# Optimization experiments

Measured on AMD Instinct MI355X. Metric: run time of the kernel, lower is better.

The kernel has to match this reference:

```python
import jax, jax.numpy as jnp
import numpy as np

H = 12        # num_heads
BLOCK = 128   # sliding-window block_size (include_adjacent=True)
EPS = 1e-5


def layer_norm(x, s, b):
    m = x.mean(-1, keepdims=True)
    v = ((x - m) ** 2).mean(-1, keepdims=True)
    return (x - m) * jax.lax.rsqrt(v + EPS) * s + b


def setup_inputs() -> dict:
    key = jax.random.key(0)
    V, D, F, L, B, S, C = 32000, 768, 3072, 4, 8, 1024, 2
    ks = jax.random.split(key, 10)
    r = lambda k, shp: jax.random.normal(k, shp, dtype=jnp.float32) * 0.02
    return {
        "tokens": jax.random.randint(ks[0], (B, S), 0, V),
        "mask": jnp.ones((B, S), dtype=jnp.int32),
        "emb": r(ks[1], (V, D)),
        "in_w": r(ks[2], (L, 3 * D, D)),
        "in_b": jnp.zeros((L, 3 * D), jnp.float32),
        "out_w": r(ks[3], (L, D, D)),
        "out_b": jnp.zeros((L, D), jnp.float32),
        "ln1_s": jnp.ones((L, D), jnp.float32),
        "ln1_b": jnp.zeros((L, D), jnp.float32),
        "ln2_s": jnp.ones((L, D), jnp.float32),
        "ln2_b": jnp.zeros((L, D), jnp.float32),
        "ff_w1": r(ks[4], (L, F, D)),
        "ff_b1": jnp.zeros((L, F), jnp.float32),
        "ff_w2": r(ks[5], (L, D, F)),
        "ff_b2": jnp.zeros((L, D), jnp.float32),
        "pool_w": r(ks[6], (1, D)),
        "pool_b": jnp.zeros((1,), jnp.float32),
        "cls_ln_s": jnp.ones((D,), jnp.float32),
        "cls_ln_b": jnp.zeros((D,), jnp.float32),
        "cls_w1": r(ks[7], (D, D)),
        "cls_b1": jnp.zeros((D,), jnp.float32),
        "cls_w2": r(ks[8], (C, D)),
        "cls_b2": jnp.zeros((C,), jnp.float32),
    }


def reference(tokens, mask, emb, in_w, in_b, out_w, out_b, ln1_s, ln1_b, ln2_s, ln2_b,
              ff_w1, ff_b1, ff_w2, ff_b2, pool_w, pool_b, cls_ln_s, cls_ln_b,
              cls_w1, cls_b1, cls_w2, cls_b2):
    B, S = tokens.shape
    D = emb.shape[1]
    L = in_w.shape[0]
    hd = D // H
    neg = jnp.finfo(jnp.float32).min

    x = emb[tokens]  # [B,S,D]
    # sinusoidal positional encoding (eval mode: dropout = identity)
    pos = jnp.arange(S, dtype=jnp.float32)[:, None]
    div = jnp.exp(jnp.arange(0, D, 2, dtype=jnp.float32) * (-np.log(10000.0) / D))
    pe = (jnp.zeros((S, D), jnp.float32)
          .at[:, 0::2].set(jnp.sin(pos * div))
          .at[:, 1::2].set(jnp.cos(pos * div)))
    x = x + pe[None]

    idx = jnp.arange(S)
    band = jnp.abs(idx[None, :] - idx[:, None]) <= BLOCK        # [S,S] allowed band
    kpm = (mask != 0)                                            # [B,S] valid keys
    allowed = band[None] & kpm[:, None, :]                       # [B,S,S]

    all_w = []
    for l in range(L):
        h = layer_norm(x, ln1_s[l], ln1_b[l])
        qkv = h @ in_w[l].T + in_b[l]                            # [B,S,3D]
        q, k, v = jnp.split(qkv, 3, axis=-1)
        q = q.reshape(B, S, H, hd).transpose(0, 2, 1, 3) * (1.0 / np.sqrt(hd))
        k = k.reshape(B, S, H, hd).transpose(0, 2, 1, 3)
        v = v.reshape(B, S, H, hd).transpose(0, 2, 1, 3)
        scores = jnp.einsum('bhqd,bhkd->bhqk', q, k)             # [B,H,S,S]
        scores = jnp.where(allowed[:, None], scores, neg)
        w = jax.nn.softmax(scores, axis=-1)
        attn = jnp.einsum('bhqk,bhkd->bhqd', w, v)
        attn = attn.transpose(0, 2, 1, 3).reshape(B, S, D)
        attn = attn @ out_w[l].T + out_b[l]
        x = x + attn
        h2 = layer_norm(x, ln2_s[l], ln2_b[l])
        ff = jax.nn.gelu(h2 @ ff_w1[l].T + ff_b1[l], approximate=False)
        ff = ff @ ff_w2[l].T + ff_b2[l]
        x = x + ff
        all_w.append(w.mean(axis=1))                             # head-averaged [B,S,S]

    # attention pooling
    sc = (x @ pool_w.T + pool_b)[..., 0]                         # [B,S]
    sc = jnp.where(mask == 0, neg, sc)
    pw = jax.nn.softmax(sc, axis=-1)[..., None]
    pooled = jnp.sum(pw * x, axis=1)                             # [B,D]
    pooled = jnp.tanh(pooled)
    c = layer_norm(pooled, cls_ln_s, cls_ln_b)
    c = jnp.tanh(c @ cls_w1.T + cls_b1)
    out = c @ cls_w2.T + cls_b2                                  # [B,2]
    return out, jnp.stack(all_w)
```

## Files before the change

### kernel.cpp

```cpp
#include <hip/hip_runtime.h>
#include <math.h>

#define S_LEN 1024
#define D_MODEL 768
#define NHEAD 12
#define NEG_INF -3.4028234663852886e38f

#define QT 32
#define KB 288

typedef _Float16 f16x8 __attribute__((ext_vector_type(8)));
typedef __attribute__((ext_vector_type(4))) float f32x4;

typedef const __attribute__((address_space(1))) unsigned int ga_u32;
typedef __attribute__((address_space(3))) unsigned int ls_u32;
__device__ __forceinline__ void gload16(const void* g, void* l) {
  __builtin_amdgcn_global_load_lds((ga_u32*)g, (ls_u32*)l, 16, 0, 0);
}

__device__ __forceinline__ float gelu_exact(float v) {
  return 0.5f * v * (1.0f + erff(v * 0.7071067811865475f));
}
__device__ __forceinline__ unsigned short f2h(float f) {
  union { _Float16 h; unsigned short u; } x; x.h = (_Float16)f; return x.u;
}

__global__ __launch_bounds__(256) void embed_kernel(
    const int* __restrict__ tok, const float* __restrict__ emb,
    float* __restrict__ X, int total) {
  int i = blockIdx.x * 256 + threadIdx.x;
  if (i >= total) return;
  int d = i % D_MODEL;
  int bs = i / D_MODEL;
  int s = bs & (S_LEN - 1);
  int t = tok[bs];
  float div = expf((float)(d & ~1) * (-9.210340371976184f / 768.0f));
  float ang = (float)s * div;
  float pe = (d & 1) ? cosf(ang) : sinf(ang);
  X[i] = emb[(size_t)t * D_MODEL + d] + pe;
}

__global__ __launch_bounds__(256) void cvt_w_h(
    const float* __restrict__ W, unsigned short* __restrict__ H, int n4) {
  int i = blockIdx.x * 256 + threadIdx.x;
  if (i >= n4) return;
  float4 w = ((const float4*)W)[i];
  ushort4 h;
  h.x = f2h(w.x); h.y = f2h(w.y); h.z = f2h(w.z); h.w = f2h(w.w);
  ((ushort4*)H)[i] = h;
}

__global__ __launch_bounds__(256) void ln_kernel(
    const float* __restrict__ X, const float* __restrict__ gam,
    const float* __restrict__ bet, unsigned short* __restrict__ Y) {
  __shared__ float scratch[4];
  const int row = blockIdx.x;
  const int tid = threadIdx.x;
  const float* xr = X + (size_t)row * D_MODEL;
  float v0 = xr[tid], v1 = xr[tid + 256], v2 = xr[tid + 512];
  float s = v0 + v1 + v2;
#pragma unroll
  for (int o = 32; o; o >>= 1) s += __shfl_xor(s, o, 64);
  if ((tid & 63) == 0) scratch[tid >> 6] = s;
  __syncthreads();
  float mean = (scratch[0] + scratch[1] + scratch[2] + scratch[3]) * (1.0f / 768.0f);
  __syncthreads();
  float d0 = v0 - mean, d1 = v1 - mean, d2 = v2 - mean;
  float ss = d0 * d0 + d1 * d1 + d2 * d2;
#pragma unroll
  for (int o = 32; o; o >>= 1) ss += __shfl_xor(ss, o, 64);
  if ((tid & 63) == 0) scratch[tid >> 6] = ss;
  __syncthreads();
  float var = (scratch[0] + scratch[1] + scratch[2] + scratch[3]) * (1.0f / 768.0f);
  float rstd = rsqrtf(var + 1e-5f);
  unsigned short* yr = Y + (size_t)row * D_MODEL;
  yr[tid]       = f2h(d0 * rstd * gam[tid]       + bet[tid]);
  yr[tid + 256] = f2h(d1 * rstd * gam[tid + 256] + bet[tid + 256]);
  yr[tid + 512] = f2h(d2 * rstd * gam[tid + 512] + bet[tid + 512]);
}

template <int EPI>
__global__ __launch_bounds__(256) void gemm128(
    const unsigned short* __restrict__ A, const unsigned short* __restrict__ W,
    const float* __restrict__ bias, unsigned short* __restrict__ C,
    int N, int K, int NX) {
  __shared__ __align__(16) unsigned short SH[24576];
  const int tid = threadIdx.x;
  const int nwg = gridDim.x;
  const int wg = ((blockIdx.x & 7) * (nwg >> 3)) + (blockIdx.x >> 3);
  const int ty = wg / NX, tx = wg - ty * NX;
  const int m0 = ty << 7, n0 = tx << 7;
  const int wave = tid >> 6, lane = tid & 63;
  const int wr = (wave >> 1) << 6, wc = (wave & 1) << 6;
  const int lq = lane >> 4, lr = lane & 15;
  const int rA0 = (wave << 5) + (lane >> 2);
  const int rA1 = rA0 + 16;
  const int sl = lane & 3;
  const size_t gA0 = (size_t)(m0 + rA0) * K + ((sl ^ ((rA0 >> 1) & 3)) << 3);
  const size_t gA1 = (size_t)(m0 + rA1) * K + ((sl ^ ((rA1 >> 1) & 3)) << 3);
  const size_t gB0 = (size_t)(n0 + rA0) * K + ((sl ^ ((rA0 >> 1) & 3)) << 3);
  const size_t gB1 = (size_t)(n0 + rA1) * K + ((sl ^ ((rA1 >> 1) & 3)) << 3);
  const int lws = wave << 10;

  const int nt = K >> 5;
  auto stage = [&](int buf, int t) {
    unsigned short* base = SH + (buf << 13);
    const int kk = t << 5;
    gload16(A + gA0 + kk, base + lws);
    gload16(A + gA1 + kk, base + lws + 512);
    gload16(W + gB0 + kk, base + 4096 + lws);
    gload16(W + gB1 + kk, base + 4096 + lws + 512);
  };
  stage(0, 0);
  stage(1, 1);

  f32x4 acc[4][4] = {};
  int cb = 0;
  for (int t = 0; t < nt; ++t) {
    if (t + 2 < nt) {
      int sb = cb + 2; if (sb >= 3) sb -= 3;
      stage(sb, t + 2);
      asm volatile("s_waitcnt vmcnt(8)" ::: "memory");
    } else if (t + 2 == nt) {
      asm volatile("s_waitcnt vmcnt(4)" ::: "memory");
    } else {
      asm volatile("s_waitcnt vmcnt(0)" ::: "memory");
    }
    __builtin_amdgcn_s_barrier();
    __builtin_amdgcn_sched_barrier(0);
    const unsigned short* As = SH + (cb << 13);
    const unsigned short* Bs = As + 4096;
    f16x8 af[4], bq[4];
#pragma unroll
    for (int i = 0; i < 4; ++i) {
      int r = wr + (i << 4) + lr;
      af[i] = *(const f16x8*)&As[r * 32 + ((lq ^ ((r >> 1) & 3)) << 3)];
    }
#pragma unroll
    for (int j = 0; j < 4; ++j) {
      int r = wc + (j << 4) + lr;
      bq[j] = *(const f16x8*)&Bs[r * 32 + ((lq ^ ((r >> 1) & 3)) << 3)];
    }
#pragma unroll
    for (int i = 0; i < 4; ++i)
#pragma unroll
      for (int j = 0; j < 4; ++j)
        acc[i][j] = __builtin_amdgcn_mfma_f32_16x16x32_f16(af[i], bq[j], acc[i][j], 0, 0, 0);
    __builtin_amdgcn_sched_barrier(0);
    __builtin_amdgcn_s_barrier();
    cb = (cb == 2) ? 0 : cb + 1;
  }
  float bval[4];
#pragma unroll
  for (int j = 0; j < 4; ++j) bval[j] = bias[n0 + wc + (j << 4) + lr];
  __syncthreads();
#pragma unroll
  for (int hh = 0; hh < 2; ++hh) {
    if ((wave >> 1) == hh) {
#pragma unroll
      for (int i = 0; i < 4; ++i)
#pragma unroll
        for (int j = 0; j < 4; ++j) {
          const int colb = wc + (j << 4) + lr;
#pragma unroll
          for (int r = 0; r < 4; ++r) {
            const int rowl = (i << 4) + (lq << 2) + r;
            float v = acc[i][j][r] + bval[j];
            if (EPI == 1) v = gelu_exact(v);
            const int ch = (colb >> 3) ^ (rowl & 7);
            SH[rowl * 128 + (ch << 3) + (colb & 7)] = f2h(v);
          }
        }
    }
    __syncthreads();
#pragma unroll
    for (int it = 0; it < 4; ++it) {
      const int cid = tid + (it << 8);
      const int row = cid >> 4, ch = cid & 15;
      uint4 v8 = *(uint4*)&SH[row * 128 + ((ch ^ (row & 7)) << 3)];
      *(uint4*)&C[(size_t)(m0 + (hh << 6) + row) * N + n0 + (ch << 3)] = v8;
    }
    __syncthreads();
  }
}

__global__ __launch_bounds__(256) void gemm64r(
    const unsigned short* __restrict__ A, const unsigned short* __restrict__ W,
    const float* __restrict__ bias, float* __restrict__ C, int N, int K, int NX) {
  __shared__ __align__(16) unsigned short SH[18432];
  const int tid = threadIdx.x;
  const int nwg = gridDim.x;
  const int wg = ((blockIdx.x & 7) * (nwg >> 3)) + (blockIdx.x >> 3);
  const int ty = wg / NX, tx = wg - ty * NX;
  const int m0 = ty << 6, n0 = tx << 7;
  const int wave = tid >> 6, lane = tid & 63;
  const int wr = (wave >> 1) << 5, wc = (wave & 1) << 6;
  const int lq = lane >> 4, lr = lane & 15;
  const int rA = (wave << 4) + (lane >> 2);
  const int rB0 = (wave << 5) + (lane >> 2);
  const int rB1 = rB0 + 16;
  const int sl = lane & 3;
  const size_t gA  = (size_t)(m0 + rA) * K + ((sl ^ ((rA >> 1) & 3)) << 3);
  const size_t gB0 = (size_t)(n0 + rB0) * K + ((sl ^ ((rB0 >> 1) & 3)) << 3);
  const size_t gB1 = (size_t)(n0 + rB1) * K + ((sl ^ ((rB1 >> 1) & 3)) << 3);
  const int lwA = wave << 9;
  const int lwB = wave << 10;

  const int nt = K >> 5;
  auto stage = [&](int buf, int t) {
    unsigned short* base = SH + buf * 6144;
    const int kk = t << 5;
    gload16(A + gA + kk, base + lwA);
    gload16(W + gB0 + kk, base + 2048 + lwB);
    gload16(W + gB1 + kk, base + 2048 + lwB + 512);
  };
  stage(0, 0);
  stage(1, 1);

  f32x4 acc[2][4] = {};
  int cb = 0;
  for (int t = 0; t < nt; ++t) {
    if (t + 2 < nt) {
      int sb = cb + 2; if (sb >= 3) sb -= 3;
      stage(sb, t + 2);
      asm volatile("s_waitcnt vmcnt(6)" ::: "memory");
    } else if (t + 2 == nt) {
      asm volatile("s_waitcnt vmcnt(3)" ::: "memory");
    } else {
      asm volatile("s_waitcnt vmcnt(0)" ::: "memory");
    }
    __builtin_amdgcn_s_barrier();
    __builtin_amdgcn_sched_barrier(0);
    const unsigned short* As = SH + cb * 6144;
    const unsigned short* Bs = As + 2048;
    f16x8 af[2], bq[4];
#pragma unroll
    for (int i = 0; i < 2; ++i) {
      int r = wr + (i << 4) + lr;
      af[i] = *(const f16x8*)&As[r * 32 + ((lq ^ ((r >> 1) & 3)) << 3)];
    }
#pragma unroll
    for (int j = 0; j < 4; ++j) {
      int r = wc + (j << 4) + lr;
      bq[j] = *(const f16x8*)&Bs[r * 32 + ((lq ^ ((r >> 1) & 3)) << 3)];
    }
#pragma unroll
    for (int i = 0; i < 2; ++i)
#pragma unroll
      for (int j = 0; j < 4; ++j)
        acc[i][j] = __builtin_amdgcn_mfma_f32_16x16x32_f16(af[i], bq[j], acc[i][j], 0, 0, 0);
    __builtin_amdgcn_sched_barrier(0);
    __builtin_amdgcn_s_barrier();
    cb = (cb == 2) ? 0 : cb + 1;
  }
#pragma unroll
  for (int j = 0; j < 4; ++j) {
    const int gcol = n0 + wc + (j << 4) + lr;
    const float bv = bias[gcol];
#pragma unroll
    for (int i = 0; i < 2; ++i) {
      const int grow0 = m0 + wr + (i << 4) + (lq << 2);
#pragma unroll
      for (int r = 0; r < 4; ++r) {
        size_t off = (size_t)(grow0 + r) * N + gcol;
        C[off] += acc[i][j][r] + bv;
      }
    }
  }
}

__global__ __launch_bounds__(512) void attn_kernel(
    const unsigned short* __restrict__ qkv, const int* __restrict__ mask,
    unsigned short* __restrict__ attn_out, float* __restrict__ allw) {
  __shared__ __align__(16) unsigned short Ks[KB * 72];
  __shared__ __align__(16) unsigned short Vt[64 * 328];
  __shared__ __align__(16) unsigned short Qs[32 * 72];
  __shared__ __align__(16) unsigned short Ps[32 * 328];
  __shared__ __align__(16) float redmax[2][16][4];
  __shared__ __align__(16) float redsum[2][16][4];
  __shared__ int kvalid[KB];

  const int qt0 = blockIdx.x * QT;
  const int b = blockIdx.y;
  const int tid = threadIdx.x;
  const int w = tid >> 6, lane = tid & 63;
  const int lr = lane & 15, lg = lane >> 4;
  const int k0 = qt0 - 128;
  const int qh = w & 1, wq = w >> 1;
  const int nkt = (wq < 2) ? 5 : 4;

  for (int j = tid; j < KB; j += 512) {
    int key = k0 + j;
    kvalid[j] = (key >= 0 && key < S_LEN && mask[b * S_LEN + key] != 0) ? 1 : 0;
  }

  f32x4 pm[5] = {};
  const size_t rowbase = (size_t)(b * S_LEN) * 2304;
  const int qloc = lg << 2;
  const int qbase = (qh << 4) + qloc;

  for (int h = 0; h < NHEAD; ++h) {
    const int hoff = h << 6;
    if (tid < 256) {
      int r = tid >> 3, c = tid & 7;
      uint4 v = *(const uint4*)(qkv + rowbase + (size_t)(qt0 + r) * 2304 + hoff + (c << 3));
      *(uint4*)&Qs[r * 72 + ((c ^ (r & 7)) << 3)] = v;
    }
    for (int idx = tid; idx < 2304; idx += 512) {
      int r = idx >> 3, c = idx & 7;
      int key = k0 + r;
      uint4 kv = {0, 0, 0, 0}, vv = {0, 0, 0, 0};
      if ((unsigned)key < (unsigned)S_LEN) {
        const unsigned short* base = qkv + rowbase + (size_t)key * 2304 + hoff + (c << 3);
        kv = *(const uint4*)(base + 768);
        vv = *(const uint4*)(base + 1536);
      }
      *(uint4*)&Ks[r * 72 + ((c ^ (r & 7)) << 3)] = kv;
      const unsigned short* ve = (const unsigned short*)&vv;
      int jc = r >> 3, jw = r & 7;
#pragma unroll
      for (int e = 0; e < 8; ++e) {
        int d = (c << 3) + e;
        Vt[d * 328 + ((jc ^ ((d >> 2) & 7)) << 3) + jw] = ve[e];
      }
    }
    __syncthreads();

    f16x8 aq[2];
#pragma unroll
    for (int kc = 0; kc < 2; ++kc) {
      int r = (qh << 4) + lr;
      aq[kc] = *(f16x8*)&Qs[r * 72 + ((((kc << 2) + lg) ^ (r & 7)) << 3)];
    }
    f32x4 sc[5];
#pragma unroll
    for (int t = 0; t < 5; ++t) {
      sc[t] = (f32x4){0.0f, 0.0f, 0.0f, 0.0f};
      if (t < nkt) {
        int r = ((wq + (t << 2)) << 4) + lr;
#pragma unroll
        for (int kc = 0; kc < 2; ++kc) {
          f16x8 bk = *(f16x8*)&Ks[r * 72 + ((((kc << 2) + lg) ^ (r & 7)) << 3)];
          sc[t] = __builtin_amdgcn_mfma_f32_16x16x32_f16(aq[kc], bk, sc[t], 0, 0, 0);
        }
      }
    }
#pragma unroll
    for (int t = 0; t < 5; ++t) if (t < nkt) {
      int j = ((wq + (t << 2)) << 4) + lr;
      int okk = kvalid[j];
#pragma unroll
      for (int rg = 0; rg < 4; ++rg) {
        int q = qbase + rg;
        float s = sc[t][rg] * 0.125f;
        sc[t][rg] = (okk && j >= q && j <= q + 256) ? s : NEG_INF;
      }
    }
    float mx[4], zs[4];
#pragma unroll
    for (int rg = 0; rg < 4; ++rg) {
      float m = NEG_INF;
#pragma unroll
      for (int t = 0; t < 5; ++t) if (t < nkt) m = fmaxf(m, sc[t][rg]);
      mx[rg] = m;
    }
#pragma unroll
    for (int o = 1; o < 16; o <<= 1)
#pragma unroll
      for (int rg = 0; rg < 4; ++rg) mx[rg] = fmaxf(mx[rg], __shfl_xor(mx[rg], o, 64));
    if (lr == 0)
#pragma unroll
      for (int rg = 0; rg < 4; ++rg) redmax[qh][qloc + rg][wq] = mx[rg];
    __syncthreads();
#pragma unroll
    for (int rg = 0; rg < 4; ++rg) {
      f32x4 v = *(f32x4*)&redmax[qh][qloc + rg][0];
      mx[rg] = fmaxf(fmaxf(v[0], v[1]), fmaxf(v[2], v[3]));
      zs[rg] = 0.0f;
    }
#pragma unroll
    for (int t = 0; t < 5; ++t) if (t < nkt)
#pragma unroll
      for (int rg = 0; rg < 4; ++rg) {
        float e = expf(sc[t][rg] - mx[rg]);
        sc[t][rg] = e;
        zs[rg] += e;
      }
#pragma unroll
    for (int o = 1; o < 16; o <<= 1)
#pragma unroll
      for (int rg = 0; rg < 4; ++rg) zs[rg] += __shfl_xor(zs[rg], o, 64);
    if (lr == 0)
#pragma unroll
      for (int rg = 0; rg < 4; ++rg) redsum[qh][qloc + rg][wq] = zs[rg];
    __syncthreads();
#pragma unroll
    for (int rg = 0; rg < 4; ++rg) {
      f32x4 v = *(f32x4*)&redsum[qh][qloc + rg][0];
      zs[rg] = 1.0f / (v[0] + v[1] + v[2] + v[3]);
    }
#pragma unroll
    for (int t = 0; t < 5; ++t) if (t < nkt) {
      int j = ((wq + (t << 2)) << 4) + lr;
      int pc = j >> 3, pw = j & 7;
#pragma unroll
      for (int rg = 0; rg < 4; ++rg) {
        float p = sc[t][rg] * zs[rg];
        pm[t][rg] += p;
        int row = qbase + rg;
        Ps[row * 328 + ((pc ^ (row & 7)) << 3) + pw] = f2h(p);
      }
    }
    __syncthreads();
    {
      const int qt = w >> 2, dt = w & 3;
      const int ra = (qt << 4) + lr;
      const int rd = (dt << 4) + lr;
      f32x4 o4 = {0.0f, 0.0f, 0.0f, 0.0f};
#pragma unroll
      for (int ks = 0; ks < 9; ++ks) {
        f16x8 pa = *(f16x8*)&Ps[ra * 328 + ((((ks << 2) + lg) ^ (ra & 7)) << 3)];
        f16x8 vb = *(f16x8*)&Vt[rd * 328 + ((((ks << 2) + lg) ^ ((rd >> 2) & 7)) << 3)];
        o4 = __builtin_amdgcn_mfma_f32_16x16x32_f16(pa, vb, o4, 0, 0, 0);
      }
      unsigned short* op = attn_out +
          ((size_t)(b * S_LEN + qt0 + (qt << 4) + (lg << 2))) * D_MODEL + hoff + (dt << 4) + lr;
#pragma unroll
      for (int rg = 0; rg < 4; ++rg) op[(size_t)rg * D_MODEL] = f2h(o4[rg]);
    }
    __syncthreads();
  }

#pragma unroll
  for (int t = 0; t < 5; ++t) if (t < nkt) {
    int j = ((wq + (t << 2)) << 4) + lr;
    int key = k0 + j;
    if ((unsigned)key < (unsigned)S_LEN) {
      float* ap = allw + ((size_t)(b * S_LEN) + qt0 + qbase) * S_LEN + key;
#pragma unroll
      for (int rg = 0; rg < 4; ++rg) ap[(size_t)rg * S_LEN] = pm[t][rg] * (1.0f / 12.0f);
    }
  }
}

__global__ __launch_bounds__(256) void pool_score(
    const float* __restrict__ X, const int* __restrict__ mask,
    const float* __restrict__ pool_w, const float* __restrict__ pool_b,
    float* __restrict__ sc) {
  const int tid = threadIdx.x;
  const int wave = tid >> 6, lane = tid & 63;
  const int row = blockIdx.x * 4 + wave;
  const float* xr = X + (size_t)row * D_MODEL;
  float acc = 0.0f;
#pragma unroll
  for (int c = 0; c < 3; ++c) {
    int d = (lane << 2) + (c << 8);
    float4 xv = *(const float4*)(xr + d);
    float4 wv = *(const float4*)(pool_w + d);
    acc += xv.x * wv.x + xv.y * wv.y + xv.z * wv.z + xv.w * wv.w;
  }
#pragma unroll
  for (int o = 32; o; o >>= 1) acc += __shfl_xor(acc, o, 64);
  if (lane == 0)
    sc[row] = (mask[row] == 0) ? NEG_INF : (acc + pool_b[0]);
}

__global__ __launch_bounds__(256) void pool_softmax(float* __restrict__ sc) {
  __shared__ float scratch[4];
  __shared__ float buf[S_LEN];
  const int b = blockIdx.x;
  const int tid = threadIdx.x;
  float* sb = sc + b * S_LEN;
  float m = NEG_INF;
  for (int s = tid; s < S_LEN; s += 256) { buf[s] = sb[s]; m = fmaxf(m, buf[s]); }
#pragma unroll
  for (int o = 32; o; o >>= 1) m = fmaxf(m, __shfl_xor(m, o, 64));
  if ((tid & 63) == 0) scratch[tid >> 6] = m;
  __syncthreads();
  m = fmaxf(fmaxf(scratch[0], scratch[1]), fmaxf(scratch[2], scratch[3]));
  __syncthreads();
  float z = 0.0f;
  for (int s = tid; s < S_LEN; s += 256) { float e = expf(buf[s] - m); buf[s] = e; z += e; }
#pragma unroll
  for (int o = 32; o; o >>= 1) z += __shfl_xor(z, o, 64);
  if ((tid & 63) == 0) scratch[tid >> 6] = z;
  __syncthreads();
  float Z = scratch[0] + scratch[1] + scratch[2] + scratch[3];
  const float inv = 1.0f / Z;
  for (int s = tid; s < S_LEN; s += 256) sb[s] = buf[s] * inv;
}

__global__ __launch_bounds__(256) void pool_sum(
    const float* __restrict__ X, const float* __restrict__ wgt,
    float* __restrict__ partial) {
  const int bx = blockIdx.x;
  const int b = blockIdx.y;
  const int dchunk = bx >> 3, schunk = bx & 7;
  const int d = (dchunk << 8) + threadIdx.x;
  const int s0 = schunk << 7;
  const float* xb = X + ((size_t)(b << 10) + s0) * D_MODEL + d;
  const float* wb = wgt + (b << 10) + s0;
  float acc = 0.0f;
  for (int s = 0; s < 128; ++s) acc += wb[s] * xb[(size_t)s * D_MODEL];
  partial[((size_t)((b << 3) + schunk)) * D_MODEL + d] = acc;
}

__global__ __launch_bounds__(256) void cls_finish(
    const float* __restrict__ partial,
    const float* __restrict__ ln_s, const float* __restrict__ ln_b,
    const float* __restrict__ w1, const float* __restrict__ b1,
    const float* __restrict__ w2, const float* __restrict__ b2,
    float* __restrict__ out) {
  const int b = blockIdx.x;
  const int tid = threadIdx.x;
  __shared__ float scratch[4];
  __shared__ __align__(16) float pbuf[D_MODEL];
  __shared__ __align__(16) float cbuf[D_MODEL];
  __shared__ __align__(16) float c1[D_MODEL];
  for (int d = tid; d < D_MODEL; d += 256) {
    float acc = 0.0f;
#pragma unroll
    for (int p = 0; p < 8; ++p) acc += partial[((size_t)((b << 3) + p)) * D_MODEL + d];
    pbuf[d] = tanhf(acc);
  }
  __syncthreads();
  float ls = 0.0f;
  for (int d = tid; d < D_MODEL; d += 256) ls += pbuf[d];
#pragma unroll
  for (int o = 32; o; o >>= 1) ls += __shfl_xor(ls, o, 64);
  if ((tid & 63) == 0) scratch[tid >> 6] = ls;
  __syncthreads();
  float mean = (scratch[0] + scratch[1] + scratch[2] + scratch[3]) * (1.0f / 768.0f);
  __syncthreads();
  float vs = 0.0f;
  for (int d = tid; d < D_MODEL; d += 256) { float dd = pbuf[d] - mean; vs += dd * dd; }
#pragma unroll
  for (int o = 32; o; o >>= 1) vs += __shfl_xor(vs, o, 64);
  if ((tid & 63) == 0) scratch[tid >> 6] = vs;
  __syncthreads();
  float var = (scratch[0] + scratch[1] + scratch[2] + scratch[3]) * (1.0f / 768.0f);
  float rstd = rsqrtf(var + 1e-5f);
  __syncthreads();
  for (int d = tid; d < D_MODEL; d += 256)
    cbuf[d] = (pbuf[d] - mean) * rstd * ln_s[d] + ln_b[d];
  __syncthreads();
  for (int i = tid; i < D_MODEL; i += 256) {
    const float* wr = w1 + (size_t)i * D_MODEL;
    float acc = 0.0f;
    for (int d = 0; d < D_MODEL; d += 4) {
      float4 wv = *(const float4*)(wr + d);
      float4 cv = *(const float4*)(&cbuf[d]);
      acc += wv.x * cv.x + wv.y * cv.y + wv.z * cv.z + wv.w * cv.w;
    }
    c1[i] = tanhf(acc + b1[i]);
  }
  __syncthreads();
#pragma unroll
  for (int jc = 0; jc < 2; ++jc) {
    float acc = 0.0f;
    for (int i = tid; i < D_MODEL; i += 256) acc += c1[i] * w2[jc * D_MODEL + i];
#pragma unroll
    for (int o = 32; o; o >>= 1) acc += __shfl_xor(acc, o, 64);
    if ((tid & 63) == 0) scratch[tid >> 6] = acc;
    __syncthreads();
    if (tid == 0) out[b * 2 + jc] = scratch[0] + scratch[1] + scratch[2] + scratch[3] + b2[jc];
    __syncthreads();
  }
}

extern "C" void kernel_launch(void* const* d_in, const int* in_sizes, int n_in,
                              void* d_out, int out_size, void* d_ws, size_t ws_size,
                              hipStream_t stream) {
  const int*   tokens  = (const int*)d_in[0];
  const int*   mask    = (const int*)d_in[1];
  const float* emb     = (const float*)d_in[2];
  const float* in_w    = (const float*)d_in[3];
  const float* in_b    = (const float*)d_in[4];
  const float* out_w   = (const float*)d_in[5];
  const float* out_b   = (const float*)d_in[6];
  const float* ln1_s   = (const float*)d_in[7];
  const float* ln1_b   = (const float*)d_in[8];
  const float* ln2_s   = (const float*)d_in[9];
  const float* ln2_b   = (const float*)d_in[10];
  const float* ff_w1   = (const float*)d_in[11];
  const float* ff_b1   = (const float*)d_in[12];
  const float* ff_w2   = (const float*)d_in[13];
  const float* ff_b2   = (const float*)d_in[14];
  const float* pool_w  = (const float*)d_in[15];
  const float* pool_b  = (const float*)d_in[16];
  const float* cls_ln_s = (const float*)d_in[17];
  const float* cls_ln_b = (const float*)d_in[18];
  const float* cls_w1  = (const float*)d_in[19];
  const float* cls_b1  = (const float*)d_in[20];
  const float* cls_w2  = (const float*)d_in[21];
  const float* cls_b2  = (const float*)d_in[22];

  float* outp = (float*)d_out;
  float* ws = (float*)d_ws;
  const size_t XN = (size_t)8 * 1024 * 768;
  const size_t BIGU = (size_t)8192 * 3072;
  float* x = ws;
  unsigned short* bigu = (unsigned short*)(ws + XN);
  unsigned short* h_f16 = (unsigned short*)(ws + XN + BIGU / 2);
  unsigned short* wall = h_f16 + XN;
  unsigned short* wall_in  = wall;
  unsigned short* wall_out = wall + (size_t)7077888;
  unsigned short* wall_ff1 = wall + (size_t)9437184;
  unsigned short* wall_ff2 = wall + (size_t)18874368;
  float* clsbuf = (float*)(wall + (size_t)28311552);
  float* sc_ws = clsbuf;
  float* partial = clsbuf + 8192;
  float* allw = outp + 16;

  hipMemsetAsync(d_out, 0, (size_t)out_size * sizeof(float), stream);

  cvt_w_h<<<6912, 256, 0, stream>>>(in_w,  wall_in,  1769472);
  cvt_w_h<<<2304, 256, 0, stream>>>(out_w, wall_out,  589824);
  cvt_w_h<<<9216, 256, 0, stream>>>(ff_w1, wall_ff1, 2359296);
  cvt_w_h<<<9216, 256, 0, stream>>>(ff_w2, wall_ff2, 2359296);

  const int total = (int)XN;
  embed_kernel<<<(total + 255) / 256, 256, 0, stream>>>(tokens, emb, x, total);

  for (int l = 0; l < 4; ++l) {
    ln_kernel<<<8192, 256, 0, stream>>>(x, ln1_s + l * 768, ln1_b + l * 768, h_f16);
    gemm128<0><<<1152, 256, 0, stream>>>(h_f16, wall_in + (size_t)l * 1769472,
                                         in_b + l * 2304, bigu, 2304, 768, 18);
    attn_kernel<<<dim3(S_LEN / QT, 8), 512, 0, stream>>>(bigu, mask, h_f16,
                                                         allw + (size_t)l * 8 * 1024 * 1024);
    gemm64r<<<768, 256, 0, stream>>>(h_f16, wall_out + (size_t)l * 589824,
                                     out_b + l * 768, x, 768, 768, 6);
    ln_kernel<<<8192, 256, 0, stream>>>(x, ln2_s + l * 768, ln2_b + l * 768, h_f16);
    gemm128<1><<<1536, 256, 0, stream>>>(h_f16, wall_ff1 + (size_t)l * 2359296,
                                         ff_b1 + l * 3072, bigu, 3072, 768, 24);
    gemm64r<<<768, 256, 0, stream>>>(bigu, wall_ff2 + (size_t)l * 2359296,
                                     ff_b2 + l * 768, x, 768, 3072, 6);
  }

  pool_score<<<2048, 256, 0, stream>>>(x, mask, pool_w, pool_b, sc_ws);
  pool_softmax<<<8, 256, 0, stream>>>(sc_ws);
  pool_sum<<<dim3(24, 8), 256, 0, stream>>>(x, sc_ws, partial);
  cls_finish<<<8, 256, 0, stream>>>(partial, cls_ln_s, cls_ln_b,
                                    cls_w1, cls_b1, cls_w2, cls_b2, outp);
}
```

Before: 1.479 ms.

## Replace 128x128 GEMM with 256x256 tile, 512-thread double-buffered kernel

QKV and FF1 projections now use a 256x256 output tile with 8 waves, a K-step of 64 and double buffering instead of a 128x128 tile with a triple-buffered K-step of 32. The larger tile raises operand reuse per LDS load and halves the barrier count per K. In exchange, 128KB of LDS limits residency to one block per CU. Grids become a few hundred blocks, which risks poor load balance and tail effects across CUs.

```diff
diff --git a/kernel.cpp b/kernel.cpp
--- a/kernel.cpp
+++ b/kernel.cpp
@@ -80,105 +80,93 @@
 }
 
 template <int EPI>
-__global__ __launch_bounds__(256) void gemm128(
+__global__ __launch_bounds__(512, 2) void gemm256(
     const unsigned short* __restrict__ A, const unsigned short* __restrict__ W,
     const float* __restrict__ bias, unsigned short* __restrict__ C,
     int N, int K, int NX) {
-  __shared__ __align__(16) unsigned short SH[24576];
+  __shared__ __align__(16) unsigned short SH[65536];
   const int tid = threadIdx.x;
   const int nwg = gridDim.x;
   const int wg = ((blockIdx.x & 7) * (nwg >> 3)) + (blockIdx.x >> 3);
   const int ty = wg / NX, tx = wg - ty * NX;
-  const int m0 = ty << 7, n0 = tx << 7;
-  const int wave = tid >> 6, lane = tid & 63;
-  const int wr = (wave >> 1) << 6, wc = (wave & 1) << 6;
+  const int m0 = ty << 8, n0 = tx << 8;
+  const int w = tid >> 6, lane = tid & 63;
+  const int wr = w >> 2, wc = w & 3;
   const int lq = lane >> 4, lr = lane & 15;
-  const int rA0 = (wave << 5) + (lane >> 2);
-  const int rA1 = rA0 + 16;
-  const int sl = lane & 3;
-  const size_t gA0 = (size_t)(m0 + rA0) * K + ((sl ^ ((rA0 >> 1) & 3)) << 3);
-  const size_t gA1 = (size_t)(m0 + rA1) * K + ((sl ^ ((rA1 >> 1) & 3)) << 3);
-  const size_t gB0 = (size_t)(n0 + rA0) * K + ((sl ^ ((rA0 >> 1) & 3)) << 3);
-  const size_t gB1 = (size_t)(n0 + rA1) * K + ((sl ^ ((rA1 >> 1) & 3)) << 3);
-  const int lws = wave << 10;
-
-  const int nt = K >> 5;
+  const int srow = tid >> 3;
+  const int scol8 = (tid & 7) ^ (srow & 7);
+  const size_t gAbase = (size_t)(m0 + srow) * K + (scol8 << 3);
+  const size_t gBbase = (size_t)(n0 + srow) * K + (scol8 << 3);
+  const int ldst = tid << 3;
+
+  const int nt = K >> 6;
   auto stage = [&](int buf, int t) {
-    unsigned short* base = SH + (buf << 13);
-    const int kk = t << 5;
-    gload16(A + gA0 + kk, base + lws);
-    gload16(A + gA1 + kk, base + lws + 512);
-    gload16(W + gB0 + kk, base + 4096 + lws);
-    gload16(W + gB1 + kk, base + 4096 + lws + 512);
+    unsigned short* bb = SH + (buf << 15);
+    const int kk = t << 6;
+#pragma unroll
+    for (int rnd = 0; rnd < 4; ++rnd) {
+      gload16(A + gAbase + (size_t)(rnd << 6) * K + kk, bb + (rnd << 12) + ldst);
+      gload16(W + gBbase + (size_t)(rnd << 6) * K + kk, bb + 16384 + (rnd << 12) + ldst);
+    }
   };
   stage(0, 0);
-  stage(1, 1);
-
-  f32x4 acc[4][4] = {};
-  int cb = 0;
+  __syncthreads();
+
+  f32x4 acc[8][4] = {};
+  int cur = 0;
   for (int t = 0; t < nt; ++t) {
-    if (t + 2 < nt) {
-      int sb = cb + 2; if (sb >= 3) sb -= 3;
-      stage(sb, t + 2);
-      asm volatile("s_waitcnt vmcnt(8)" ::: "memory");
-    } else if (t + 2 == nt) {
-      asm volatile("s_waitcnt vmcnt(4)" ::: "memory");
-    } else {
-      asm volatile("s_waitcnt vmcnt(0)" ::: "memory");
-    }
-    __builtin_amdgcn_s_barrier();
-    __builtin_amdgcn_sched_barrier(0);
-    const unsigned short* As = SH + (cb << 13);
-    const unsigned short* Bs = As + 4096;
-    f16x8 af[4], bq[4];
-#pragma unroll
-    for (int i = 0; i < 4; ++i) {
-      int r = wr + (i << 4) + lr;
-      af[i] = *(const f16x8*)&As[r * 32 + ((lq ^ ((r >> 1) & 3)) << 3)];
-    }
-#pragma unroll
-    for (int j = 0; j < 4; ++j) {
-      int r = wc + (j << 4) + lr;
-      bq[j] = *(const f16x8*)&Bs[r * 32 + ((lq ^ ((r >> 1) & 3)) << 3)];
-    }
-#pragma unroll
-    for (int i = 0; i < 4; ++i)
-#pragma unroll
-      for (int j = 0; j < 4; ++j)
-        acc[i][j] = __builtin_amdgcn_mfma_f32_16x16x32_f16(af[i], bq[j], acc[i][j], 0, 0, 0);
-    __builtin_amdgcn_sched_barrier(0);
-    __builtin_amdgcn_s_barrier();
-    cb = (cb == 2) ? 0 : cb + 1;
-  }
+    if (t + 1 < nt) stage(cur ^ 1, t + 1);
+    const unsigned short* As = SH + (cur << 15);
+    const unsigned short* Bs = As + 16384;
+#pragma unroll
+    for (int s = 0; s < 2; ++s) {
+      f16x8 bq[4];
+#pragma unroll
+      for (int j = 0; j < 4; ++j) {
+        int rb = (wc << 6) + (j << 4) + lr;
+        bq[j] = *(const f16x8*)&Bs[(rb << 6) + ((((s << 2) + lq) ^ (rb & 7)) << 3)];
+      }
+#pragma unroll
+      for (int i = 0; i < 8; ++i) {
+        int ra = (wr << 7) + (i << 4) + lr;
+        f16x8 av = *(const f16x8*)&As[(ra << 6) + ((((s << 2) + lq) ^ (ra & 7)) << 3)];
+#pragma unroll
+        for (int j = 0; j < 4; ++j)
+          acc[i][j] = __builtin_amdgcn_mfma_f32_16x16x32_f16(av, bq[j], acc[i][j], 0, 0, 0);
+      }
+    }
+    __syncthreads();
+    cur ^= 1;
+  }
+
   float bval[4];
 #pragma unroll
-  for (int j = 0; j < 4; ++j) bval[j] = bias[n0 + wc + (j << 4) + lr];
-  __syncthreads();
+  for (int j = 0; j < 4; ++j) bval[j] = bias[n0 + (wc << 6) + (j << 4) + lr];
 #pragma unroll
   for (int hh = 0; hh < 2; ++hh) {
-    if ((wave >> 1) == hh) {
-#pragma unroll
-      for (int i = 0; i < 4; ++i)
+    if (wr == hh) {
+#pragma unroll
+      for (int i = 0; i < 8; ++i)
 #pragma unroll
         for (int j = 0; j < 4; ++j) {
-          const int colb = wc + (j << 4) + lr;
-#pragma unroll
-          for (int r = 0; r < 4; ++r) {
-            const int rowl = (i << 4) + (lq << 2) + r;
-            float v = acc[i][j][r] + bval[j];
+          const int col = (wc << 6) + (j << 4) + lr;
+          const int chx = col >> 3, clo = col & 7;
+#pragma unroll
+          for (int rg = 0; rg < 4; ++rg) {
+            const int rowl = (i << 4) + (lq << 2) + rg;
+            float v = acc[i][j][rg] + bval[j];
             if (EPI == 1) v = gelu_exact(v);
-            const int ch = (colb >> 3) ^ (rowl & 7);
-            SH[rowl * 128 + (ch << 3) + (colb & 7)] = f2h(v);
+            SH[(rowl << 8) + ((chx ^ (rowl & 7)) << 3) + clo] = f2h(v);
           }
         }
     }
     __syncthreads();
 #pragma unroll
-    for (int it = 0; it < 4; ++it) {
-      const int cid = tid + (it << 8);
-      const int row = cid >> 4, ch = cid & 15;
-      uint4 v8 = *(uint4*)&SH[row * 128 + ((ch ^ (row & 7)) << 3)];
-      *(uint4*)&C[(size_t)(m0 + (hh << 6) + row) * N + n0 + (ch << 3)] = v8;
+    for (int it = 0; it < 8; ++it) {
+      const int cid = tid + (it << 9);
+      const int row = cid >> 5, ch = cid & 31;
+      uint4 v8 = *(uint4*)&SH[(row << 8) + ((ch ^ (row & 7)) << 3)];
+      *(uint4*)&C[(size_t)(m0 + (hh << 7) + row) * N + n0 + (ch << 3)] = v8;
     }
     __syncthreads();
   }
@@ -624,15 +612,15 @@
 
   for (int l = 0; l < 4; ++l) {
     ln_kernel<<<8192, 256, 0, stream>>>(x, ln1_s + l * 768, ln1_b + l * 768, h_f16);
-    gemm128<0><<<1152, 256, 0, stream>>>(h_f16, wall_in + (size_t)l * 1769472,
-                                         in_b + l * 2304, bigu, 2304, 768, 18);
+    gemm256<0><<<288, 512, 0, stream>>>(h_f16, wall_in + (size_t)l * 1769472,
+                                        in_b + l * 2304, bigu, 2304, 768, 9);
     attn_kernel<<<dim3(S_LEN / QT, 8), 512, 0, stream>>>(bigu, mask, h_f16,
                                                          allw + (size_t)l * 8 * 1024 * 1024);
     gemm64r<<<768, 256, 0, stream>>>(h_f16, wall_out + (size_t)l * 589824,
                                      out_b + l * 768, x, 768, 768, 6);
     ln_kernel<<<8192, 256, 0, stream>>>(x, ln2_s + l * 768, ln2_b + l * 768, h_f16);
-    gemm128<1><<<1536, 256, 0, stream>>>(h_f16, wall_ff1 + (size_t)l * 2359296,
-                                         ff_b1 + l * 3072, bigu, 3072, 768, 24);
+    gemm256<1><<<384, 512, 0, stream>>>(h_f16, wall_ff1 + (size_t)l * 2359296,
+                                        ff_b1 + l * 3072, bigu, 3072, 768, 12);
     gemm64r<<<768, 256, 0, stream>>>(bigu, wall_ff2 + (size_t)l * 2359296,
                                      ff_b2 + l * 768, x, 768, 3072, 6);
   }
```

Result: slower. 1.603 ms (+8.4%).
